# Optimization experiments

Measured on AMD Instinct MI355X. Metric: run time of the kernel, lower is better.

The kernel has to match this reference:

```python
import jax, jax.numpy as jnp
import numpy as np


def setup_inputs() -> dict:
    key = jax.random.key(0)
    x = jax.random.normal(key, (64, 256, 56, 56), dtype=jnp.float32)
    return {"x": x}


def reference(x):
    # Per-sample (over all dims except batch) min/max fake-quantization,
    # then dequantize, then hardtanh(0, 6) == ReLU6.
    B = x.shape[0]
    xf = x.reshape(B, -1)
    m = xf.min(axis=1).reshape((B,) + (1,) * (x.ndim - 1))  # per-sample min
    M = xf.max(axis=1).reshape((B,) + (1,) * (x.ndim - 1))  # per-sample max
    rng = M - m
    q = jnp.round(254.0 * (x - m) / rng - 127.0) / 1000.0
    y = (1000.0 * q + 127.0) * rng / 254.0 + m
    return jnp.clip(y, 0.0, 6.0)
```

## Files before the change

### kernel.cpp

```cpp
#include <hip/hip_runtime.h>
#include <hip/hip_bf16.h>
#include <math.h>


#define SAMPLE_V4   200704
#define BPS_R       49
#define V4_PER_BLK_R 4096
#define BPS_E       98
#define V4_PER_BLK_E 2048
#define NSAMPLES    64

__global__ __launch_bounds__(256) void qr_reduce(const float4* __restrict__ x,
                                                 float* __restrict__ pmin,
                                                 float* __restrict__ pmax) {
    const int s = blockIdx.x / BPS_R;
    const int b = blockIdx.x % BPS_R;
    const float4* base = x + (size_t)s * SAMPLE_V4 + (size_t)b * V4_PER_BLK_R;

    float mn = INFINITY, mx = -INFINITY;
    for (int i = threadIdx.x; i < V4_PER_BLK_R; i += 256) {
        float4 v = base[i];
        mn = fminf(mn, fminf(fminf(v.x, v.y), fminf(v.z, v.w)));
        mx = fmaxf(mx, fmaxf(fmaxf(v.x, v.y), fmaxf(v.z, v.w)));
    }
    #pragma unroll
    for (int off = 32; off > 0; off >>= 1) {
        mn = fminf(mn, __shfl_down(mn, off, 64));
        mx = fmaxf(mx, __shfl_down(mx, off, 64));
    }
    __shared__ float smn[4], smx[4];
    const int wave = threadIdx.x >> 6;
    if ((threadIdx.x & 63) == 0) { smn[wave] = mn; smx[wave] = mx; }
    __syncthreads();
    if (threadIdx.x == 0) {
        mn = fminf(fminf(smn[0], smn[1]), fminf(smn[2], smn[3]));
        mx = fmaxf(fmaxf(smx[0], smx[1]), fmaxf(smx[2], smx[3]));
        pmin[blockIdx.x] = mn;
        pmax[blockIdx.x] = mx;
    }
}

__global__ __launch_bounds__(64) void qr_finalize(const float* __restrict__ pmin,
                                                  const float* __restrict__ pmax,
                                                  float* __restrict__ params) {
    const int s = blockIdx.x;
    const int t = threadIdx.x;
    float mn = (t < BPS_R) ? pmin[s * BPS_R + t] : INFINITY;
    float mx = (t < BPS_R) ? pmax[s * BPS_R + t] : -INFINITY;
    #pragma unroll
    for (int off = 32; off > 0; off >>= 1) {
        mn = fminf(mn, __shfl_down(mn, off, 64));
        mx = fmaxf(mx, __shfl_down(mx, off, 64));
    }
    if (t == 0) {
        const float rng = mx - mn;
        params[s * 3 + 0] = mn;
        params[s * 3 + 1] = rng * (1.0f / 254.0f);
        params[s * 3 + 2] = 254.0f / rng;
    }
}

__device__ __forceinline__ float qr_apply1(float x, float m, float sc, float inv) {
    float k = rintf((x - m) * inv - 127.0f);
    float y = fmaf(k + 127.0f, sc, m);
    return fminf(fmaxf(y, 0.0f), 6.0f);
}

__global__ __launch_bounds__(256) void qr_apply(const float4* __restrict__ x,
                                                float4* __restrict__ y,
                                                const float* __restrict__ params) {
    const int s = blockIdx.x / BPS_E;
    const int b = blockIdx.x % BPS_E;
    const float m   = params[s * 3 + 0];
    const float sc  = params[s * 3 + 1];
    const float inv = params[s * 3 + 2];
    const size_t off = (size_t)s * SAMPLE_V4 + (size_t)b * V4_PER_BLK_E;
    const float4* xb = x + off;
    float4* yb = y + off;
    for (int i = threadIdx.x; i < V4_PER_BLK_E; i += 256) {
        float4 v = xb[i];
        v.x = qr_apply1(v.x, m, sc, inv);
        v.y = qr_apply1(v.y, m, sc, inv);
        v.z = qr_apply1(v.z, m, sc, inv);
        v.w = qr_apply1(v.w, m, sc, inv);
        yb[i] = v;
    }
}

extern "C" void kernel_launch(void* const* d_in, const int* in_sizes, int n_in,
                              void* d_out, int out_size, void* d_ws, size_t ws_size,
                              hipStream_t stream) {
    const float* x = (const float*)d_in[0];
    float* out = (float*)d_out;

    float* pmin   = (float*)d_ws;
    float* pmax   = pmin + NSAMPLES * BPS_R;
    float* params = pmax + NSAMPLES * BPS_R;

    qr_reduce<<<NSAMPLES * BPS_R, 256, 0, stream>>>((const float4*)x, pmin, pmax);
    qr_finalize<<<NSAMPLES, 64, 0, stream>>>(pmin, pmax, params);
    qr_apply<<<NSAMPLES * BPS_E, 256, 0, stream>>>((const float4*)x, (float4*)out, params);
}
```

Before: 378.0 us.

## Fold finalize into apply kernel, shrink reduce grid, use nontemporal stores

Removes the separate finalize launch; each apply block now reduces the per-sample partial min/max itself and computes the quant params into shared memory. The reduce grid shrinks to 16 blocks per sample with larger per-block spans, so there are fewer partials to combine. Output stores become nontemporal to avoid cache pollution. Fewer blocks in the reduce may lower memory-level parallelism, and every apply block repeats a small redundant reduction.

Result: no change. 370.6 us (-1.9%).

```diff
diff --git a/kernel.cpp b/kernel.cpp
--- a/kernel.cpp
+++ b/kernel.cpp
@@ -3,18 +3,20 @@
 #include <math.h>
 
 
-#define SAMPLE_V4   200704
-#define BPS_R       49
-#define V4_PER_BLK_R 4096
-#define BPS_E       98
+#define SAMPLE_V4    200704
+#define NSAMPLES     64
+#define BPS_R        16
+#define V4_PER_BLK_R 12544
+#define BPS_E        98
 #define V4_PER_BLK_E 2048
-#define NSAMPLES    64
+
+typedef __attribute__((ext_vector_type(4))) float fvec4;
 
 __global__ __launch_bounds__(256) void qr_reduce(const float4* __restrict__ x,
                                                  float* __restrict__ pmin,
                                                  float* __restrict__ pmax) {
-    const int s = blockIdx.x / BPS_R;
-    const int b = blockIdx.x % BPS_R;
+    const int s = blockIdx.x >> 4;
+    const int b = blockIdx.x & (BPS_R - 1);
     const float4* base = x + (size_t)s * SAMPLE_V4 + (size_t)b * V4_PER_BLK_R;
 
     float mn = INFINITY, mx = -INFINITY;
@@ -33,30 +35,8 @@
     if ((threadIdx.x & 63) == 0) { smn[wave] = mn; smx[wave] = mx; }
     __syncthreads();
     if (threadIdx.x == 0) {
-        mn = fminf(fminf(smn[0], smn[1]), fminf(smn[2], smn[3]));
-        mx = fmaxf(fmaxf(smx[0], smx[1]), fmaxf(smx[2], smx[3]));
-        pmin[blockIdx.x] = mn;
-        pmax[blockIdx.x] = mx;
-    }
-}
-
-__global__ __launch_bounds__(64) void qr_finalize(const float* __restrict__ pmin,
-                                                  const float* __restrict__ pmax,
-                                                  float* __restrict__ params) {
-    const int s = blockIdx.x;
-    const int t = threadIdx.x;
-    float mn = (t < BPS_R) ? pmin[s * BPS_R + t] : INFINITY;
-    float mx = (t < BPS_R) ? pmax[s * BPS_R + t] : -INFINITY;
-    #pragma unroll
-    for (int off = 32; off > 0; off >>= 1) {
-        mn = fminf(mn, __shfl_down(mn, off, 64));
-        mx = fmaxf(mx, __shfl_down(mx, off, 64));
-    }
-    if (t == 0) {
-        const float rng = mx - mn;
-        params[s * 3 + 0] = mn;
-        params[s * 3 + 1] = rng * (1.0f / 254.0f);
-        params[s * 3 + 2] = 254.0f / rng;
+        pmin[blockIdx.x] = fminf(fminf(smn[0], smn[1]), fminf(smn[2], smn[3]));
+        pmax[blockIdx.x] = fmaxf(fmaxf(smx[0], smx[1]), fmaxf(smx[2], smx[3]));
     }
 }
 
@@ -68,22 +48,41 @@
 
 __global__ __launch_bounds__(256) void qr_apply(const float4* __restrict__ x,
                                                 float4* __restrict__ y,
-                                                const float* __restrict__ params) {
+                                                const float* __restrict__ pmin,
+                                                const float* __restrict__ pmax) {
     const int s = blockIdx.x / BPS_E;
     const int b = blockIdx.x % BPS_E;
-    const float m   = params[s * 3 + 0];
-    const float sc  = params[s * 3 + 1];
-    const float inv = params[s * 3 + 2];
+
+    __shared__ float sp[3];
+    if (threadIdx.x < 64) {
+        float mn = (threadIdx.x < BPS_R) ? pmin[s * BPS_R + threadIdx.x] : INFINITY;
+        float mx = (threadIdx.x < BPS_R) ? pmax[s * BPS_R + threadIdx.x] : -INFINITY;
+        #pragma unroll
+        for (int off = 8; off > 0; off >>= 1) {
+            mn = fminf(mn, __shfl_down(mn, off, 64));
+            mx = fmaxf(mx, __shfl_down(mx, off, 64));
+        }
+        if (threadIdx.x == 0) {
+            const float rng = mx - mn;
+            sp[0] = mn;
+            sp[1] = rng * (1.0f / 254.0f);
+            sp[2] = 254.0f / rng;
+        }
+    }
+    __syncthreads();
+    const float m = sp[0], sc = sp[1], inv = sp[2];
+
     const size_t off = (size_t)s * SAMPLE_V4 + (size_t)b * V4_PER_BLK_E;
     const float4* xb = x + off;
-    float4* yb = y + off;
+    fvec4* yb = (fvec4*)(y + off);
     for (int i = threadIdx.x; i < V4_PER_BLK_E; i += 256) {
         float4 v = xb[i];
-        v.x = qr_apply1(v.x, m, sc, inv);
-        v.y = qr_apply1(v.y, m, sc, inv);
-        v.z = qr_apply1(v.z, m, sc, inv);
-        v.w = qr_apply1(v.w, m, sc, inv);
-        yb[i] = v;
+        fvec4 o;
+        o.x = qr_apply1(v.x, m, sc, inv);
+        o.y = qr_apply1(v.y, m, sc, inv);
+        o.z = qr_apply1(v.z, m, sc, inv);
+        o.w = qr_apply1(v.w, m, sc, inv);
+        __builtin_nontemporal_store(o, &yb[i]);
     }
 }
 
@@ -93,11 +92,10 @@
     const float* x = (const float*)d_in[0];
     float* out = (float*)d_out;
 
-    float* pmin   = (float*)d_ws;
-    float* pmax   = pmin + NSAMPLES * BPS_R;
-    float* params = pmax + NSAMPLES * BPS_R;
+    float* pmin = (float*)d_ws;
+    float* pmax = pmin + NSAMPLES * BPS_R;
 
     qr_reduce<<<NSAMPLES * BPS_R, 256, 0, stream>>>((const float4*)x, pmin, pmax);
-    qr_finalize<<<NSAMPLES, 64, 0, stream>>>(pmin, pmax, params);
-    qr_apply<<<NSAMPLES * BPS_E, 256, 0, stream>>>((const float4*)x, (float4*)out, params);
+    qr_apply<<<NSAMPLES * BPS_E, 256, 0, stream>>>((const float4*)x, (float4*)out,
+                                                   pmin, pmax);
 }
```
